# Kernel tuning notes

Measured on AMD Instinct MI355X. Metric: run time of the kernel, lower is better.

The kernel has to match this reference:

```python
import jax, jax.numpy as jnp
import numpy as np

INPUT_SIZE = 10
HIDDEN_SIZE = 20
T, B = 512, 4096


def setup_inputs() -> dict:
    key = jax.random.key(0)
    ks = jax.random.split(key, 7)
    # PyTorch LSTMCell init: uniform(-k, k), k = 1/sqrt(hidden_size)
    k = 1.0 / np.sqrt(HIDDEN_SIZE)
    u = lambda kk, shape: jax.random.uniform(kk, shape, jnp.float32, -k, k)
    return {
        "input_sequence": jax.random.normal(ks[0], (T, B, INPUT_SIZE), jnp.float32),
        "initial_h": jax.random.normal(ks[1], (B, HIDDEN_SIZE), jnp.float32),
        "initial_c": jax.random.normal(ks[2], (B, HIDDEN_SIZE), jnp.float32),
        "W_ih": u(ks[3], (4 * HIDDEN_SIZE, INPUT_SIZE)),
        "W_hh": u(ks[4], (4 * HIDDEN_SIZE, HIDDEN_SIZE)),
        "b_ih": u(ks[5], (4 * HIDDEN_SIZE,)),
        "b_hh": u(ks[6], (4 * HIDDEN_SIZE,)),
    }


def _lstm_scan(input_sequence, initial_h, initial_c, W_ih, W_hh, b_ih, b_hh):
    H = initial_h.shape[-1]
    # Precompute input projections for all timesteps in one big GEMM:
    # [T, B, 4H] = [T, B, I] @ [I, 4H]
    x_proj = jnp.einsum("tbi,gi->tbg", input_sequence, W_ih) + b_ih + b_hh

    def step(carry, xg):
        h, c = carry
        gates = xg + h @ W_hh.T  # [B, 4H]
        i, f, g, o = jnp.split(gates, 4, axis=-1)  # PyTorch gate order i,f,g,o
        i = jax.nn.sigmoid(i)
        f = jax.nn.sigmoid(f)
        g = jnp.tanh(g)
        o = jax.nn.sigmoid(o)
        c_new = f * c + i * g
        h_new = o * jnp.tanh(c_new)
        return (h_new, c_new), h_new

    (h, c), outputs = jax.lax.scan(step, (initial_h, initial_c), x_proj)
    return outputs, h, c


def reference(input_sequence, initial_h, initial_c, W_ih, W_hh, b_ih, b_hh):
    return _lstm_scan(input_sequence, initial_h, initial_c, W_ih, W_hh, b_ih, b_hh)
```

## Files before the change

### kernel.cpp

```cpp
#include <hip/hip_runtime.h>


#define T_STEPS 512
#define BATCH   4096
#define ISZ     10
#define HSZ     20
#define BPB     3

#if defined(__has_builtin)
#if __has_builtin(__builtin_amdgcn_exp2f)
#define FAST_EXP2(x) __builtin_amdgcn_exp2f(x)
#endif
#if __has_builtin(__builtin_amdgcn_rcpf)
#define FAST_RCP(x) __builtin_amdgcn_rcpf(x)
#endif
#endif
#ifndef FAST_EXP2
#define FAST_EXP2(x) exp2f(x)
#endif
#ifndef FAST_RCP
#define FAST_RCP(x) (1.0f/(x))
#endif

__device__ __forceinline__ float sigm_f(float x) {
    return FAST_RCP(1.0f + FAST_EXP2(x * -1.4426950408889634f));
}
__device__ __forceinline__ float tanh_f(float x) {
    return 2.0f * FAST_RCP(1.0f + FAST_EXP2(x * -2.8853900817779268f)) - 1.0f;
}

__global__ __launch_bounds__(64, 2) void lstm_fused_kernel(
    const float* __restrict__ x,
    const float* __restrict__ h0,
    const float* __restrict__ c0,
    const float* __restrict__ Wih,
    const float* __restrict__ Whh,
    const float* __restrict__ bih,
    const float* __restrict__ bhh,
    float* __restrict__ out)
{
    __shared__ __align__(16) float hbuf[BPB][24];

    const int tid = threadIdx.x;
    const int b   = tid / HSZ;
    const int j   = tid % HSZ;
    const int gb  = blockIdx.x * BPB + b;
    if (tid >= BPB * HSZ || gb >= BATCH) return;

    float w[4][ISZ + HSZ];
    float bias[4];
#pragma unroll
    for (int r = 0; r < 4; ++r) {
        const int row = r * HSZ + j;
#pragma unroll
        for (int k = 0; k < ISZ; ++k) w[r][k] = Wih[row * ISZ + k];
#pragma unroll
        for (int k = 0; k < HSZ; ++k) w[r][ISZ + k] = Whh[row * HSZ + k];
        bias[r] = bih[row] + bhh[row];
    }

    float c = c0[(size_t)gb * HSZ + j];
    hbuf[b][j] = h0[(size_t)gb * HSZ + j];

    const float* xbase = x + (size_t)gb * ISZ;
    float* outp = out + (size_t)gb * HSZ + j;

    float2 nx[5];
    {
        const float2* xp = (const float2*)xbase;
#pragma unroll
        for (int q = 0; q < 5; ++q) nx[q] = xp[q];
    }

    float hn = hbuf[b][j];
    for (int t = 0; t < T_STEPS; ++t) {
        float cx[ISZ];
#pragma unroll
        for (int q = 0; q < 5; ++q) { cx[2*q] = nx[q].x; cx[2*q+1] = nx[q].y; }
        if (t + 1 < T_STEPS) {
            const float2* xp = (const float2*)(xbase + (size_t)(t + 1) * BATCH * ISZ);
#pragma unroll
            for (int q = 0; q < 5; ++q) nx[q] = xp[q];
        }

        float hreg[HSZ];
        const float4* hrow = (const float4*)(&hbuf[b][0]);
#pragma unroll
        for (int q = 0; q < 5; ++q) {
            float4 v = hrow[q];
            hreg[4*q+0] = v.x; hreg[4*q+1] = v.y;
            hreg[4*q+2] = v.z; hreg[4*q+3] = v.w;
        }

        float acc[4];
#pragma unroll
        for (int r = 0; r < 4; ++r) {
            float a0 = bias[r], a1 = 0.0f;
#pragma unroll
            for (int k = 0; k < ISZ; k += 2) {
                a0 += w[r][k]     * cx[k];
                a1 += w[r][k + 1] * cx[k + 1];
            }
#pragma unroll
            for (int k = 0; k < HSZ; k += 2) {
                a0 += w[r][ISZ + k]     * hreg[k];
                a1 += w[r][ISZ + k + 1] * hreg[k + 1];
            }
            acc[r] = a0 + a1;
        }

        const float ig = sigm_f(acc[0]);
        const float fg = sigm_f(acc[1]);
        const float gg = tanh_f(acc[2]);
        const float og = sigm_f(acc[3]);
        c  = fg * c + ig * gg;
        hn = og * tanh_f(c);

        hbuf[b][j] = hn;
        outp[(size_t)t * (BATCH * HSZ)] = hn;
    }

    const size_t tail = (size_t)T_STEPS * BATCH * HSZ;
    out[tail + (size_t)gb * HSZ + j] = hn;
    out[tail + (size_t)BATCH * HSZ + (size_t)gb * HSZ + j] = c;
}

extern "C" void kernel_launch(void* const* d_in, const int* in_sizes, int n_in,
                              void* d_out, int out_size, void* d_ws, size_t ws_size,
                              hipStream_t stream) {
    const float* x   = (const float*)d_in[0];
    const float* h0  = (const float*)d_in[1];
    const float* c0  = (const float*)d_in[2];
    const float* Wih = (const float*)d_in[3];
    const float* Whh = (const float*)d_in[4];
    const float* bih = (const float*)d_in[5];
    const float* bhh = (const float*)d_in[6];
    float* out = (float*)d_out;

    const int nblk = (BATCH + BPB - 1) / BPB;
    lstm_fused_kernel<<<nblk, 64, 0, stream>>>(x, h0, c0, Wih, Whh, bih, bhh, out);
}
```

Measured before the change: 550.9 us.

## Use packed FMA, deeper x prefetch, and move input projection off the critical path

The cell math now uses two-wide vector FMAs (packed fp32), with weights stored as float2 pairs. The x prefetch is deepened to 4 timesteps in a rotating register buffer. Each step computes the input-projection part before loading the next x, so that work sits outside the h dependency chain. The LDS row is padded to 22 and read as float2, and occupancy hint is dropped to 1, which gives more registers at the cost of fewer resident waves.

```diff
diff --git a/kernel.cpp b/kernel.cpp
--- a/kernel.cpp
+++ b/kernel.cpp
@@ -6,6 +6,14 @@
 #define ISZ     10
 #define HSZ     20
 #define BPB     3
+#define PF      4
+#define LDSPAD  22
+
+typedef float v2f __attribute__((ext_vector_type(2)));
+
+__device__ __forceinline__ v2f fma2(v2f a, v2f b, v2f c) {
+    return __builtin_elementwise_fma(a, b, c);
+}
 
 #if defined(__has_builtin)
 #if __has_builtin(__builtin_amdgcn_exp2f)
@@ -29,7 +37,7 @@
     return 2.0f * FAST_RCP(1.0f + FAST_EXP2(x * -2.8853900817779268f)) - 1.0f;
 }
 
-__global__ __launch_bounds__(64, 2) void lstm_fused_kernel(
+__global__ __launch_bounds__(64, 1) void lstm_fused_kernel(
     const float* __restrict__ x,
     const float* __restrict__ h0,
     const float* __restrict__ c0,
@@ -39,7 +47,7 @@
     const float* __restrict__ bhh,
     float* __restrict__ out)
 {
-    __shared__ __align__(16) float hbuf[BPB][24];
+    __shared__ __align__(8) float hbuf[BPB][LDSPAD];
 
     const int tid = threadIdx.x;
     const int b   = tid / HSZ;
@@ -47,15 +55,17 @@
     const int gb  = blockIdx.x * BPB + b;
     if (tid >= BPB * HSZ || gb >= BATCH) return;
 
-    float w[4][ISZ + HSZ];
+    v2f wv[4][15];
     float bias[4];
 #pragma unroll
     for (int r = 0; r < 4; ++r) {
         const int row = r * HSZ + j;
+        const v2f* wi = (const v2f*)(Wih + row * ISZ);
+        const v2f* wh = (const v2f*)(Whh + row * HSZ);
 #pragma unroll
-        for (int k = 0; k < ISZ; ++k) w[r][k] = Wih[row * ISZ + k];
+        for (int k = 0; k < 5; ++k)  wv[r][k] = wi[k];
 #pragma unroll
-        for (int k = 0; k < HSZ; ++k) w[r][ISZ + k] = Whh[row * HSZ + k];
+        for (int k = 0; k < 10; ++k) wv[r][5 + k] = wh[k];
         bias[r] = bih[row] + bhh[row];
     }
 
@@ -65,59 +75,57 @@
     const float* xbase = x + (size_t)gb * ISZ;
     float* outp = out + (size_t)gb * HSZ + j;
 
-    float2 nx[5];
-    {
-        const float2* xp = (const float2*)xbase;
+    v2f nx[PF][5];
 #pragma unroll
-        for (int q = 0; q < 5; ++q) nx[q] = xp[q];
+    for (int p = 0; p < PF; ++p) {
+        const v2f* xp = (const v2f*)(xbase + (size_t)p * BATCH * ISZ);
+#pragma unroll
+        for (int q = 0; q < 5; ++q) nx[p][q] = xp[q];
     }
 
+    const v2f* hrow = (const v2f*)(&hbuf[b][0]);
     float hn = hbuf[b][j];
-    for (int t = 0; t < T_STEPS; ++t) {
-        float cx[ISZ];
+
+    for (int tb = 0; tb < T_STEPS; tb += PF) {
 #pragma unroll
-        for (int q = 0; q < 5; ++q) { cx[2*q] = nx[q].x; cx[2*q+1] = nx[q].y; }
-        if (t + 1 < T_STEPS) {
-            const float2* xp = (const float2*)(xbase + (size_t)(t + 1) * BATCH * ISZ);
+        for (int u = 0; u < PF; ++u) {
+            const int t = tb + u;
+
+            v2f hv[10];
 #pragma unroll
-            for (int q = 0; q < 5; ++q) nx[q] = xp[q];
+            for (int q = 0; q < 10; ++q) hv[q] = hrow[q];
+
+            v2f a[4];
+#pragma unroll
+            for (int r = 0; r < 4; ++r) {
+                a[r] = (v2f){bias[r], 0.0f};
+#pragma unroll
+                for (int k = 0; k < 5; ++k) a[r] = fma2(wv[r][k], nx[u][k], a[r]);
+            }
+
+            {
+                int tp = t + PF; if (tp > T_STEPS - 1) tp = T_STEPS - 1;
+                const v2f* xp = (const v2f*)(xbase + (size_t)tp * BATCH * ISZ);
+#pragma unroll
+                for (int q = 0; q < 5; ++q) nx[u][q] = xp[q];
+            }
+
+#pragma unroll
+            for (int r = 0; r < 4; ++r) {
+#pragma unroll
+                for (int k = 0; k < 10; ++k) a[r] = fma2(wv[r][5 + k], hv[k], a[r]);
+            }
+
+            const float ig = sigm_f(a[0].x + a[0].y);
+            const float fg = sigm_f(a[1].x + a[1].y);
+            const float gg = tanh_f(a[2].x + a[2].y);
+            const float og = sigm_f(a[3].x + a[3].y);
+            c  = fg * c + ig * gg;
+            hn = og * tanh_f(c);
+
+            hbuf[b][j] = hn;
+            outp[(size_t)t * (BATCH * HSZ)] = hn;
         }
-
-        float hreg[HSZ];
-        const float4* hrow = (const float4*)(&hbuf[b][0]);
-#pragma unroll
-        for (int q = 0; q < 5; ++q) {
-            float4 v = hrow[q];
-            hreg[4*q+0] = v.x; hreg[4*q+1] = v.y;
-            hreg[4*q+2] = v.z; hreg[4*q+3] = v.w;
-        }
-
-        float acc[4];
-#pragma unroll
-        for (int r = 0; r < 4; ++r) {
-            float a0 = bias[r], a1 = 0.0f;
-#pragma unroll
-            for (int k = 0; k < ISZ; k += 2) {
-                a0 += w[r][k]     * cx[k];
-                a1 += w[r][k + 1] * cx[k + 1];
-            }
-#pragma unroll
-            for (int k = 0; k < HSZ; k += 2) {
-                a0 += w[r][ISZ + k]     * hreg[k];
-                a1 += w[r][ISZ + k + 1] * hreg[k + 1];
-            }
-            acc[r] = a0 + a1;
-        }
-
-        const float ig = sigm_f(acc[0]);
-        const float fg = sigm_f(acc[1]);
-        const float gg = tanh_f(acc[2]);
-        const float og = sigm_f(acc[3]);
-        c  = fg * c + ig * gg;
-        hn = og * tanh_f(c);
-
-        hbuf[b][j] = hn;
-        outp[(size_t)t * (BATCH * HSZ)] = hn;
     }
 
     const size_t tail = (size_t)T_STEPS * BATCH * HSZ;
```

Measured after the change: 476.7 us. 13.5% less time.
